# Performance work log

Measured on AMD Instinct MI355X. Metric: run time of the kernel, lower is better.

## Reference

```python
import jax, jax.numpy as jnp
import numpy as np

B, CIN, T, H, W = 4, 64, 8, 32, 32
COUT, AHID = 64, 16
HWF = H * W


def _conv2d(x, w, b):
    y = jax.lax.conv_general_dilated(x, w, (1, 1), [(1, 1), (1, 1)],
                                     dimension_numbers=("NCHW", "OIHW", "NCHW"))
    return y + b[None, :, None, None]


def _conv1x1(x, w, b):
    return jnp.einsum("bchw,oc->bohw", x, w) + b[None, :, None, None]


def setup_inputs():
    key = jax.random.key(0)
    ks = jax.random.split(key, 18)
    s = 0.05
    d = {}
    d["X"] = jax.random.normal(ks[0], (B, CIN, T, H, W), jnp.float32)
    d["conv_w"] = jax.random.normal(ks[1], (4 * COUT, CIN + COUT, 3, 3), jnp.float32) * s
    d["conv_b"] = jnp.zeros((4 * COUT,), jnp.float32)
    d["W_ci"] = jax.random.normal(ks[2], (COUT, H, W), jnp.float32) * s
    d["W_cf"] = jax.random.normal(ks[3], (COUT, H, W), jnp.float32) * s
    d["W_co"] = jax.random.normal(ks[4], (COUT, H, W), jnp.float32) * s
    d["q_w"] = jax.random.normal(ks[5], (AHID, COUT), jnp.float32) * s
    d["q_b"] = jnp.zeros((AHID,), jnp.float32)
    d["k_w"] = jax.random.normal(ks[6], (AHID, COUT), jnp.float32) * s
    d["k_b"] = jnp.zeros((AHID,), jnp.float32)
    d["k2_w"] = jax.random.normal(ks[7], (AHID, COUT), jnp.float32) * s
    d["k2_b"] = jnp.zeros((AHID,), jnp.float32)
    d["v_w"] = jax.random.normal(ks[8], (COUT, COUT), jnp.float32) * s
    d["v_b"] = jnp.zeros((COUT,), jnp.float32)
    d["v2_w"] = jax.random.normal(ks[9], (COUT, COUT), jnp.float32) * s
    d["v2_b"] = jnp.zeros((COUT,), jnp.float32)
    d["z_w"] = jax.random.normal(ks[10], (2 * COUT, 2 * COUT), jnp.float32) * s
    d["z_b"] = jnp.zeros((2 * COUT,), jnp.float32)
    d["m_w"] = jax.random.normal(ks[11], (3 * COUT, 3 * COUT), jnp.float32) * s
    d["m_b"] = jnp.zeros((3 * COUT,), jnp.float32)
    return d


def _forward(X, conv_w, conv_b, W_ci, W_cf, W_co, q_w, q_b, k_w, k_b, k2_w, k2_b,
             v_w, v_b, v2_w, v2_b, z_w, z_b, m_w, m_b):
    def step(carry, x_t):
        h, c, m = carry
        # ConvLSTM cell with peephole connections
        gates = _conv2d(jnp.concatenate([x_t, h], axis=1), conv_w, conv_b)
        i_c, f_c, g_c, o_c = jnp.split(gates, 4, axis=1)
        ig = jax.nn.sigmoid(i_c + W_ci * c)
        fg = jax.nn.sigmoid(f_c + W_cf * c)
        c_new = fg * c + ig * jnp.tanh(g_c)
        og = jax.nn.sigmoid(o_c + W_co * c_new)
        h_new = og * jnp.tanh(c_new)
        # Self-attention memory module (all projections are 1x1 convs)
        q = _conv1x1(h_new, q_w, q_b).reshape(B, AHID, HWF)
        kh = _conv1x1(h_new, k_w, k_b).reshape(B, AHID, HWF)
        vh = _conv1x1(h_new, v_w, v_b).reshape(B, COUT, HWF)
        km = _conv1x1(m, k2_w, k2_b).reshape(B, AHID, HWF)
        vm = _conv1x1(m, v2_w, v2_b).reshape(B, COUT, HWF)
        att_h = jax.nn.softmax(jnp.einsum("ban,bam->bnm", q, kh), axis=-1)  # (B,HW,HW)
        att_m = jax.nn.softmax(jnp.einsum("ban,bam->bnm", q, km), axis=-1)
        z_h = jnp.einsum("bnm,bcm->bcn", att_h, vh)  # (B,COUT,HW)
        z_m = jnp.einsum("bnm,bcm->bcn", att_m, vm)
        z = jnp.concatenate([z_h, z_m], axis=1).reshape(B, 2 * COUT, H, W)
        z = _conv1x1(z, z_w, z_b)
        comb = _conv1x1(jnp.concatenate([z, h_new], axis=1), m_w, m_b)
        mo, mg, mi = jnp.split(comb, 3, axis=1)
        gi = jax.nn.sigmoid(mi)
        m_new = (1.0 - gi) * m + gi * jnp.tanh(mg)
        h_out = jax.nn.sigmoid(mo) * m_new
        return (h_out, c_new, m_new), h_out

    zeros = jnp.zeros((B, COUT, H, W), X.dtype)
    Xs = jnp.moveaxis(X, 2, 0)  # (T, B, CIN, H, W)
    _, hs = jax.lax.scan(step, (zeros, zeros, zeros), Xs)
    return jnp.moveaxis(hs, 0, 2)  # (B, COUT, T, H, W)


def reference(X, conv_w, conv_b, W_ci, W_cf, W_co, q_w, q_b, k_w, k_b, k2_w, k2_b,
              v_w, v_b, v2_w, v2_b, z_w, z_b, m_w, m_b):
    return _forward(X, conv_w, conv_b, W_ci, W_cf, W_co, q_w, q_b, k_w, k_b,
                    k2_w, k2_b, v_w, v_b, v2_w, v2_b, z_w, z_b, m_w, m_b)
```

## Files before the change

### kernel.cpp

```cpp
#include <hip/hip_runtime.h>
#include <hip/hip_bf16.h>

typedef __hip_bfloat16 bf16;
typedef unsigned short ushort;
typedef __attribute__((ext_vector_type(8))) short short8v;
typedef __attribute__((ext_vector_type(4))) float float4v;

__device__ __forceinline__ float b2f(bf16 v){ return __bfloat162float(v); }
__device__ __forceinline__ float sigm(float x){ return 1.0f/(1.0f+__expf(-x)); }
__device__ __forceinline__ float tanhc(float x){
  x = fminf(15.0f, fmaxf(-15.0f, x));
  float e = __expf(2.0f*x);
  return (e-1.0f)/(e+1.0f);
}
__device__ __forceinline__ ushort f2bu(float f){
  bf16 h = __float2bfloat16(f); return *reinterpret_cast<ushort*>(&h);
}
__device__ __forceinline__ float bu2f(ushort u){
  return __uint_as_float(((unsigned)u)<<16);
}
__device__ __forceinline__ short8v ldfrag(const ushort* p){
  return *reinterpret_cast<const short8v*>(p);
}
__device__ __forceinline__ void glds16(const ushort* g, ushort* l){
// ... 112 lines not shown

__global__ __launch_bounds__(256) void k_init(const void* __restrict__ conv_w,
                                              const int* __restrict__ flagp,
                                              float* __restrict__ ws){
  int i = blockIdx.x*256 + threadIdx.x;
  int flag = *flagp;
  if (i < 786432) ws[WS_H + i] = 0.0f;
  if (i < 32) ws[WS_ZROW + i] = 0.0f;
  if (i < 196608) ((unsigned*)(ws + WS_QB16))[i] = 0u;
  if (i < 294912){
    int ci = i & 127;
    int j = i >> 7;
    int mm = j & 255, p = j >> 8;
    int cc = mm >> 2, g = mm & 3;
    int si = ((g*64 + cc)*128 + ci)*9 + p;
    float f;
    ushort hi, lo = 0;
    if (flag){
      f = ((const float*)conv_w)[si];
      hi = f2bu(f);
      lo = f2bu(f - bu2f(hi));
    } else {
      hi = ((const ushort*)conv_w)[si];
    }
    if (ci < 64){
      int di = (j << 6) + ((((ci >> 3) ^ (mm & 7)) << 3) | (ci & 7));
      ((ushort*)(ws + WS_WXAH))[di] = hi;
      ((ushort*)(ws + WS_WXAL))[di] = lo;
    } else {
      int c2 = ci - 64;
      int di = (j << 6) + ((((c2 >> 3) ^ (mm & 7)) << 3) | (c2 & 7));
      ((ushort*)(ws + WS_WHAH))[di] = hi;
      ((ushort*)(ws + WS_WHAL))[di] = lo;
    }
  }
  if (i < 131072){
    ((unsigned*)(ws + WS_HTHI))[i] = 0u;
    ((unsigned*)(ws + WS_HTLO))[i] = 0u;
    ((unsigned*)(ws + WS_MTH))[i] = 0u;
    ((unsigned*)(ws + WS_MTL))[i] = 0u;
  }
}

__global__ __launch_bounds__(256) void k_xt(const void* __restrict__ Xraw,
                                            const int* __restrict__ flagp,
                                            float* __restrict__ ws){
  __shared__ ushort hi_s[64][66];
  __shared__ ushort lo_s[64][66];
  int pt = blockIdx.x, s = blockIdx.y;
  int b = s >> 3, t = s & 7;
  int flag = *flagp;
  int tid = threadIdx.x;
  for (int k = 0; k < 16; ++k){
    int idx = tid + k*256;
    int ci = idx >> 6, pxl = idx & 63;
    size_t si = ((size_t)(b*64 + ci)*8 + t)*1024 + pt*64 + pxl;
    if (flag){
      float f = ((const float*)Xraw)[si];
      ushort h = f2bu(f);
      hi_s[pxl][ci] = h;
      lo_s[pxl][ci] = f2bu(f - bu2f(h));
    } else {
      hi_s[pxl][ci] = ((const ushort*)Xraw)[si];
    }
  }
  __syncthreads();
  ushort* xh = (ushort*)(ws + WS_XTHI) + ((size_t)s*1024 + pt*64)*64;
  ushort* xl = (ushort*)(ws + WS_XTLO) + ((size_t)s*1024 + pt*64)*64;
  for (int k = 0; k < 16; ++k){
    int idx = tid + k*256;
    int pxl = idx >> 6, ci = idx & 63;
    xh[pxl*64 + ci] = hi_s[pxl][ci];
    if (flag) xl[pxl*64 + ci] = lo_s[pxl][ci];
  }
}

__global__ __launch_bounds__(512, 4) void k_convx(
  const int* __restrict__ flagp,
  const ushort* __restrict__ wxah, const ushort* __restrict__ wxal,
  const ushort* __restrict__ xt_hi, const ushort* __restrict__ xt_lo,
  float* __restrict__ gxg, ushort* __restrict__ gxo)
{
  __shared__ ushort xabuf[8192];
  __shared__ ushort xsm[54*136];
  int nt = blockIdx.x, mh = blockIdx.y, tb = blockIdx.z;
  int tid = threadIdx.x;
  int flag = *flagp;
  int ytile = nt >> 1, x0 = (nt & 1) * 16;
  const ushort* xb  = xt_hi + (size_t)tb*65536;
  const ushort* xlb = xt_lo + (size_t)tb*65536;
  int w = tid >> 6, lane = tid & 63, lr = lane & 15, lk = lane >> 4;
  const ushort* aw  = wxah + (size_t)(mh*128 + w*16)*64 + lane*8;
  const ushort* awl = wxal + (size_t)(mh*128 + w*16)*64 + lane*8;
  ushort* areg = xabuf + w*1024;

  const uint4 Z16 = make_uint4(0,0,0,0);
  for (int idx = tid; idx < 864; idx += 512){
    int slot = idx >> 4, c = idx & 15;
    int rr = slot / 18, xi = slot - rr*18;
    int gy = ytile - 1 + rr, gx2 = x0 - 1 + xi;
    bool valid = (gy >= 0) & (gy < 32) & (gx2 >= 0) & (gx2 < 32);
    int px = gy*32 + gx2;
    uint4 v = Z16;
    if (valid){
      if (c < 8)       v = *reinterpret_cast<const uint4*>(xb  + (size_t)px*64 + c*8);
      else if (flag)   v = *reinterpret_cast<const uint4*>(xlb + (size_t)px*64 + (c-8)*8);
    }
    *reinterpret_cast<uint4*>(&xsm[slot*136 + c*8]) = v;
  }
  __syncthreads();

  int px = nt*16 + lr;
  int sw = lr & 7;
  const int cx0 = ((lk ^ sw) << 3);
  const int cx1 = (((4+lk) ^ sw) << 3);
  float4v acc = {0.f,0.f,0.f,0.f};

  #pragma unroll 1
  for (int p = 0; p < 9; ++p){
    glds16(aw + (size_t)p*16384,       areg);
    glds16(aw + (size_t)p*16384 + 512, areg + 512);
    asm volatile("s_waitcnt vmcnt(0)" ::: "memory");
    __builtin_amdgcn_sched_barrier(0);
    short8v A0 = ldfrag(areg + lr*64 + cx0);
    short8v A1 = ldfrag(areg + lr*64 + cx1);
    int pinl = (p/3)*18 + lr + (p%3);
    const ushort* bl = &xsm[pinl*136 + lk*8];
    short8v BX0 = ldfrag(bl), BX1 = ldfrag(bl+32);
    acc = __builtin_amdgcn_mfma_f32_16x16x32_bf16(A0, BX0, acc, 0,0,0);
    acc = __builtin_amdgcn_mfma_f32_16x16x32_bf16(A1, BX1, acc, 0,0,0);
    if (flag){
      short8v BXl0 = ldfrag(bl+64), BXl1 = ldfrag(bl+96);
      acc = __builtin_amdgcn_mfma_f32_16x16x32_bf16(A0, BXl0, acc, 0,0,0);
      acc = __builtin_amdgcn_mfma_f32_16x16x32_bf16(A1, BXl1, acc, 0,0,0);
      asm volatile("s_waitcnt lgkmcnt(0)" ::: "memory");
      __builtin_amdgcn_sched_barrier(0);
      glds16(awl + (size_t)p*16384,       areg);
      glds16(awl + (size_t)p*16384 + 512, areg + 512);
      asm volatile("s_waitcnt vmcnt(0)" ::: "memory");
      __builtin_amdgcn_sched_barrier(0);
      short8v Al0 = ldfrag(areg + lr*64 + cx0);
      short8v Al1 = ldfrag(areg + lr*64 + cx1);
      acc = __builtin_amdgcn_mfma_f32_16x16x32_bf16(Al0, BX0, acc, 0,0,0);
      acc = __builtin_amdgcn_mfma_f32_16x16x32_bf16(Al1, BX1, acc, 0,0,0);
      asm volatile("s_waitcnt lgkmcnt(0)" ::: "memory");
      __builtin_amdgcn_sched_barrier(0);
    } else {
      asm volatile("s_waitcnt lgkmcnt(0)" ::: "memory");
      __builtin_amdgcn_sched_barrier(0);
    }
  }

  {
    int cc = mh*32 + w*4 + lk;
    gxg[((size_t)tb*64 + cc)*1024 + px] = acc[2];
    ushort* go = gxo + ((size_t)tb*192 + cc*3)*1024 + px;
    go[0]    = f2bu(acc[0]);
    go[1024] = f2bu(acc[1]);
    go[2048] = f2bu(acc[3]);
  }
}

__global__ __launch_bounds__(512, 4) void k_conv_mfma(
  const int* __restrict__ flagp,
  const ushort* __restrict__ whah, const ushort* __restrict__ whal,
  const ushort* __restrict__ ht_hi, const ushort* __restrict__ ht_lo,
  const float* __restrict__ gxg, const ushort* __restrict__ gxo,
  const float* __restrict__ smalls, float* __restrict__ cst,
  ushort* __restrict__ hnth, ushort* __restrict__ hntl, int t)
{
  __shared__ ushort albuf[16384];
  __shared__ ushort bsm[54*136];
  int nt = blockIdx.x, mh = blockIdx.y, b = blockIdx.z;
  int tid = threadIdx.x;
  int flag = *flagp;
  int ytile = nt >> 1, x0 = (nt & 1) * 16;

  const ushort* hb  = ht_hi + (size_t)b*65536;
  const ushort* hlb = ht_lo + (size_t)b*65536;

  int w = tid >> 6, lane = tid & 63, lr = lane & 15, lk = lane >> 4;
  const ushort* aw  = whah + (size_t)(mh*128 + w*16)*64 + lane*8;
  const ushort* awl = whal + (size_t)(mh*128 + w*16)*64 + lane*8;
  ushort* areg = albuf + w*1024;
  ushort* aregl = albuf + 8192 + w*1024;

  if (!flag){
    glds16(aw, areg);
    glds16(aw + 512, areg + 512);
  }

  int px = nt*16 + lr;
  int cc = mh*32 + w*4 + lk;
  int tb = b*8 + t;
  const ushort* go = gxo + ((size_t)tb*192 + cc*3)*1024 + px;
  float a0 = bu2f(go[0]);
  float a1 = bu2f(go[1024]);
  float a3 = bu2f(go[2048]);
  float a2 = gxg[((size_t)tb*64 + cc)*1024 + px];

  const uint4 Z16 = make_uint4(0,0,0,0);
  for (int idx = tid; idx < 864; idx += 512){
    int slot = idx >> 4, c = idx & 15;
    int rr = slot / 18, xi = slot - rr*18;
    int gy = ytile - 1 + rr, gx2 = x0 - 1 + xi;
    bool valid = (gy >= 0) & (gy < 32) & (gx2 >= 0) & (gx2 < 32);
    int hpx = gy*32 + gx2;
    uint4 v = Z16;
    if (valid){
      if (c < 8) v = *reinterpret_cast<const uint4*>(hb  + (size_t)hpx*64 + c*8);
      else       v = *reinterpret_cast<const uint4*>(hlb + (size_t)hpx*64 + (c-8)*8);
    }
    *reinterpret_cast<uint4*>(&bsm[slot*136 + c*8]) = v;
  }
  __syncthreads();

  const int sw = lr & 7;
  const int c2n = ((lk ^ sw) << 3);
  const int c3n = (((4+lk) ^ sw) << 3);

  float4v acc = {a0, a1, a2, a3};

  if (!flag){
    #pragma unroll
    for (int p = 0; p < 9; ++p){
      if (p > 0){
        asm volatile("s_waitcnt vmcnt(0)" ::: "memory");
        __builtin_amdgcn_sched_barrier(0);
      }
      short8v A2 = ldfrag(areg + lr*64 + c2n);
      short8v A3 = ldfrag(areg + lr*64 + c3n);
      if (p < 8){
        asm volatile("s_waitcnt lgkmcnt(0)" ::: "memory");
        __builtin_amdgcn_sched_barrier(0);
        glds16(aw + (size_t)(p+1)*16384,       areg);
        glds16(aw + (size_t)(p+1)*16384 + 512, areg + 512);
        __builtin_amdgcn_sched_barrier(0);
      }
      int pinl = (p/3)*18 + lr + (p%3);
      const ushort* bl = &bsm[pinl*136 + lk*8];
      short8v BH0 = ldfrag(bl),    BH1 = ldfrag(bl+32);
      short8v BL0 = ldfrag(bl+64), BL1 = ldfrag(bl+96);
      acc = __builtin_amdgcn_mfma_f32_16x16x32_bf16(A2, BH0, acc, 0,0,0);
      acc = __builtin_amdgcn_mfma_f32_16x16x32_bf16(A3, BH1, acc, 0,0,0);
      acc = __builtin_amdgcn_mfma_f32_16x16x32_bf16(A2, BL0, acc, 0,0,0);
      acc = __builtin_amdgcn_mfma_f32_16x16x32_bf16(A3, BL1, acc, 0,0,0);
    }
  } else {
    #pragma unroll 1
    for (int p = 0; p < 9; ++p){
      glds16(aw + (size_t)p*16384,       areg);
      glds16(aw + (size_t)p*16384 + 512, areg + 512);
      glds16(awl + (size_t)p*16384,       aregl);
      glds16(awl + (size_t)p*16384 + 512, aregl + 512);
      asm volatile("s_waitcnt vmcnt(0)" ::: "memory");
      __builtin_amdgcn_sched_barrier(0);
      short8v A2 = ldfrag(areg + lr*64 + c2n);
      short8v A3 = ldfrag(areg + lr*64 + c3n);
      short8v Al2 = ldfrag(aregl + lr*64 + c2n);
      short8v Al3 = ldfrag(aregl + lr*64 + c3n);
      int pinl = (p/3)*18 + lr + (p%3);
      const ushort* bl = &bsm[pinl*136 + lk*8];
      short8v BH0 = ldfrag(bl),    BH1 = ldfrag(bl+32);
      short8v BL0 = ldfrag(bl+64), BL1 = ldfrag(bl+96);
      acc = __builtin_amdgcn_mfma_f32_16x16x32_bf16(A2, BH0, acc, 0,0,0);
      acc = __builtin_amdgcn_mfma_f32_16x16x32_bf16(A3, BH1, acc, 0,0,0);
      acc = __builtin_amdgcn_mfma_f32_16x16x32_bf16(A2, BL0, acc, 0,0,0);
      acc = __builtin_amdgcn_mfma_f32_16x16x32_bf16(A3, BL1, acc, 0,0,0);
      acc = __builtin_amdgcn_mfma_f32_16x16x32_bf16(Al2, BH0, acc, 0,0,0);
      acc = __builtin_amdgcn_mfma_f32_16x16x32_bf16(Al3, BH1, acc, 0,0,0);
      asm volatile("s_waitcnt lgkmcnt(0)" ::: "memory");
      __builtin_amdgcn_sched_barrier(0);
    }
  }

  {
    int wi = cc*1024 + px;
    size_t sidx = ((size_t)(b*64 + cc))*1024 + px;
    float cprev = cst[sidx];
    float ic = acc[0] + smalls[O_CB + cc];
    float fc = acc[1] + smalls[O_CB + 64 + cc];
    float gc = acc[2] + smalls[O_CB + 128 + cc];
    float oc = acc[3] + smalls[O_CB + 192 + cc];
    float ig = sigm(ic + smalls[O_WCI + wi]*cprev);
    float fg = sigm(fc + smalls[O_WCF + wi]*cprev);
    float cnew = fg*cprev + ig*tanhc(gc);
    float og = sigm(oc + smalls[O_WCO + wi]*cnew);
    cst[sidx] = cnew;
    float hv = og*tanhc(cnew);
    size_t tix = ((size_t)b*1024 + px)*64 + cc;
    ushort hh = f2bu(hv);
    hnth[tix] = hh;
    hntl[tix] = f2bu(hv - bu2f(hh));
  }
}

__global__ __launch_bounds__(256) void k_projm(
  const ushort* __restrict__ hnth, const ushort* __restrict__ hntl,
  const ushort* __restrict__ mth, const ushort* __restrict__ mtl,
  const ushort* __restrict__ pwh, const ushort* __restrict__ pwl,
  const float* __restrict__ smalls, const int* __restrict__ flagp,
  ushort* __restrict__ qb16, ushort* __restrict__ khb16, ushort* __restrict__ kmb16,
  ushort* __restrict__ vth16, ushort* __restrict__ vtm16)
{
  int nt = blockIdx.x, b = blockIdx.y;
  int n0 = nt*16;
  int tid = threadIdx.x;
  int w = tid >> 6, lane = tid & 63, lr = lane & 15, lk = lane >> 4;
  int flag = *flagp;
  const float4v Z4 = {0.f,0.f,0.f,0.f};
  size_t bb = ((size_t)b*1024 + n0 + lr)*64 + lk*8;
  short8v BH0  = ldfrag(hnth + bb), BH1  = ldfrag(hnth + bb + 32);
  short8v BHl0 = ldfrag(hntl + bb), BHl1 = ldfrag(hntl + bb + 32);
  short8v BM0  = ldfrag(mth + bb),  BM1  = ldfrag(mth + bb + 32);
  short8v BMl0 = ldfrag(mtl + bb),  BMl1 = ldfrag(mtl + bb + 32);
  int n = n0 + lr;
  int tstart = w*3;
  int tcnt = (w == 3) ? 2 : 3;
  for (int ti = 0; ti < tcnt; ++ti){
    int tt = tstart + ti;
    const ushort* ar = pwh + (size_t)(tt*16 + lr)*64 + lk*8;
    short8v a0 = ldfrag(ar), a1 = ldfrag(ar + 32);
    bool srcm = (tt == 2) || (tt >= 7);
    short8v b0  = srcm ? BM0  : BH0,  b1  = srcm ? BM1  : BH1;
    short8v bl0 = srcm ? BMl0 : BHl0, bl1 = srcm ? BMl1 : BHl1;
    float4v d = Z4;
    d = __builtin_amdgcn_mfma_f32_16x16x32_bf16(a0, b0,  d, 0,0,0);
    d = __builtin_amdgcn_mfma_f32_16x16x32_bf16(a1, b1,  d, 0,0,0);
    d = __builtin_amdgcn_mfma_f32_16x16x32_bf16(a0, bl0, d, 0,0,0);
    d = __builtin_amdgcn_mfma_f32_16x16x32_bf16(a1, bl1, d, 0,0,0);
    if (flag){
      const ushort* arl = pwl + (size_t)(tt*16 + lr)*64 + lk*8;
      short8v al0 = ldfrag(arl), al1 = ldfrag(arl + 32);
      d = __builtin_amdgcn_mfma_f32_16x16x32_bf16(al0, b0, d, 0,0,0);
      d = __builtin_amdgcn_mfma_f32_16x16x32_bf16(al1, b1, d, 0,0,0);
    }
    int boff = (tt==0) ? O_QB : (tt==1) ? O_KB : (tt==2) ? O_K2B
             : (tt<7) ? (O_VB + (tt-3)*16) : (O_V2B + (tt-7)*16);
    if (tt < 3){
      ushort* base = (tt==0) ? qb16 : (tt==1) ? khb16 : kmb16;
      ushort u[4];
      #pragma unroll
      for (int q = 0; q < 4; ++q)
        u[q] = f2bu(d[q] + smalls[boff + lk*4 + q]);
      *reinterpret_cast<uint2*>(&base[((size_t)b*1024 + n)*32 + lk*4]) =
        make_uint2((unsigned)u[0] | ((unsigned)u[1]<<16),
                   (unsigned)u[2] | ((unsigned)u[3]<<16));
    } else {
      ushort* base = (tt<7) ? vth16 : vtm16;
      int cc0 = ((tt<7) ? (tt-3) : (tt-7))*16 + lk*4;
      #pragma unroll
      for (int q = 0; q < 4; ++q)
        base[((size_t)b*64 + cc0 + q)*1024 + n] = f2bu(d[q] + smalls[boff + lk*4 + q]);
    }
  }
}

__global__ __launch_bounds__(512) void k_fattz(
  const ushort* __restrict__ qb16, const ushort* __restrict__ khb16,
  const ushort* __restrict__ kmb16, const ushort* __restrict__ vth16,
  const ushort* __restrict__ vtm16,
  const ushort* __restrict__ hnth, const ushort* __restrict__ hntl,
  const float* __restrict__ smalls,
  const ushort* __restrict__ zw16h, const ushort* __restrict__ zw16l,
  const ushort* __restrict__ mw16h, const ushort* __restrict__ mw16l,
  const int* __restrict__ flagp,
  float* __restrict__ mst, ushort* __restrict__ mth, ushort* __restrict__ mtl,
  ushort* __restrict__ hth, ushort* __restrict__ htl,
  void* __restrict__ outraw, int t)
{
  __shared__ __align__(16) unsigned char poolA[17408];
  __shared__ __align__(16) ushort ztbh[16*136];
  __shared__ __align__(16) ushort ztbl[16*136];
  __shared__ float cb[192*17];
  __shared__ float ml[64*17];
  __shared__ float rs_s[2][4][16];

  ushort* es   = (ushort*)poolA;
  ushort* zbh  = (ushort*)poolA;
  ushort* zbl  = (ushort*)(poolA + 8704);
  float*  ho_s = (float*)poolA;
  float*  mn_s = (float*)(poolA + 4352);

  int nt = blockIdx.x, b = blockIdx.y;
  int n0 = nt*16;
  int tid = threadIdx.x;
  int w = tid >> 6, lane = tid & 63, lr = lane & 15, lk = lane >> 4;
  int br = w >> 2, wq = w & 3;
  int flag = *flagp;
  const float4v Z4 = {0.f,0.f,0.f,0.f};

  const ushort* kb = (br ? kmb16 : khb16) + (size_t)b*32768;
  const ushort* vt = (br ? vtm16 : vth16) + (size_t)b*65536;
  const ushort* qp = qb16 + (size_t)b*32768;
  ushort* esb = es + br*4352;

  for (int idx = tid; idx < 1024; idx += 512){
    int ch = idx >> 4, pp = idx & 15;
    ml[ch*17+pp] = mst[((size_t)b*64 + ch)*1024 + n0 + pp];
  }

  short8v qf = ldfrag(qp + (size_t)(n0 + lr)*32 + lk*8);

  float4v acc[2];
  acc[0]=Z4; acc[1]=Z4;
  float rsum = 0.f;

  #pragma unroll 1
  for (int mc = 0; mc < 4; ++mc){
    int mbase = mc*256 + wq*64;
    #pragma unroll
    for (int tau = 0; tau < 4; ++tau){
      short8v af = ldfrag(kb + (size_t)(mbase + tau*16 + lr)*32 + lk*8);
      float4v d = __builtin_amdgcn_mfma_f32_16x16x32_bf16(af, qf, Z4, 0,0,0);
      ushort u0 = f2bu(__expf(fminf(d[0], 60.f)));
      ushort u1 = f2bu(__expf(fminf(d[1], 60.f)));
      ushort u2 = f2bu(__expf(fminf(d[2], 60.f)));
      ushort u3 = f2bu(__expf(fminf(d[3], 60.f)));
      rsum += (bu2f(u0) + bu2f(u1)) + (bu2f(u2) + bu2f(u3));
// ... 126 lines not shown
    for (int q = 0; q < 4; ++q)
      cb[(r0+q)*17 + lr] = cacc[q] + smalls[O_MB + r0 + q];
  }
  __syncthreads();

  {
    int px = tid >> 5, lr2 = tid & 31;
    #pragma unroll
    for (int j = 0; j < 2; ++j){
      int ch = lr2 + 32*j;
      float mo = cb[ch*17 + px];
      float mg = cb[(64+ch)*17 + px];
      float mi = cb[(128+ch)*17 + px];
      float mold = ml[ch*17 + px];
      float gi = sigm(mi);
      float mnew = (1.0f-gi)*mold + gi*tanhc(mg);
      float ho = sigm(mo)*mnew;
      ho_s[ch*17+px] = ho;
      mn_s[ch*17+px] = mnew;
    }
  }
  __syncthreads();
  for (int idx = tid; idx < 1024; idx += 512){
    int ch = idx >> 4, pp = idx & 15;
    int n = n0 + pp;
    size_t gidx = ((size_t)b*64 + ch)*1024 + n;
    float mn = mn_s[ch*17+pp];
    mst[gidx] = mn;
    float ho = ho_s[ch*17+pp];
    size_t tix = ((size_t)b*1024 + n)*64 + ch;
    ushort hb_ = f2bu(ho);
    hth[tix] = hb_;
    htl[tix] = f2bu(ho - bu2f(hb_));
    ushort mh_ = f2bu(mn);
    mth[tix] = mh_;
    mtl[tix] = f2bu(mn - bu2f(mh_));
    size_t oidx = ((size_t)(b*64+ch)*8 + t)*1024 + n;
    if (flag) ((float*)outraw)[oidx] = ho;
    else      ((bf16*)outraw)[oidx] = __float2bfloat16(ho);
  }
}

extern "C" void kernel_launch(void* const* d_in, const int* in_sizes, int n_in,
                              void* d_out, int out_size, void* d_ws, size_t ws_size,
                              hipStream_t stream)
{
  float* ws = (float*)d_ws;
  int* flag = (int*)(ws + WS_FLAG);
  float* c    = ws + WS_C;
  float* m    = ws + WS_M;
  float* gxg  = ws + WS_GXG;
  ushort* gxo   = (ushort*)(ws + WS_GXO);
  ushort* qb16  = (ushort*)(ws + WS_QB16);
  ushort* khb16 = (ushort*)(ws + WS_KHB16);
  ushort* kmb16 = (ushort*)(ws + WS_KMB16);
  ushort* vth16 = (ushort*)(ws + WS_VTH16);
  ushort* vtm16 = (ushort*)(ws + WS_VTM16);
  ushort* mth   = (ushort*)(ws + WS_MTH);
  ushort* mtl   = (ushort*)(ws + WS_MTL);
  ushort* hnth  = (ushort*)(ws + WS_HNTH);
  ushort* hntl  = (ushort*)(ws + WS_HNTL);
  ushort* zw16h = (ushort*)(ws + WS_ZW16H);
  ushort* zw16l = (ushort*)(ws + WS_ZW16L);
  ushort* mw16h = (ushort*)(ws + WS_MW16H);
  ushort* mw16l = (ushort*)(ws + WS_MW16L);
  ushort* wxah  = (ushort*)(ws + WS_WXAH);
  ushort* wxal  = (ushort*)(ws + WS_WXAL);
  ushort* whah  = (ushort*)(ws + WS_WHAH);
  ushort* whal  = (ushort*)(ws + WS_WHAL);
  ushort* xt_hi = (ushort*)(ws + WS_XTHI);
  ushort* xt_lo = (ushort*)(ws + WS_XTLO);
  ushort* ht_hi = (ushort*)(ws + WS_HTHI);
  ushort* ht_lo = (ushort*)(ws + WS_HTLO);
  ushort* pwh   = (ushort*)(ws + WS_PWH);
  ushort* pwl   = (ushort*)(ws + WS_PWL);

  k_probe<<<1, 256, 0, stream>>>((const unsigned int*)d_in[0], flag);
  P18 pk;
  for (int i = 0; i < 18; ++i) pk.p[i] = d_in[2 + i];
  k_wconv<<<dim3(64,18), 256, 0, stream>>>(pk, flag, ws);
  k_init<<<3072, 256, 0, stream>>>(d_in[1], flag, ws);
  k_xt<<<dim3(16,32), 256, 0, stream>>>(d_in[0], flag, ws);
  k_wtrans<<<144, 256, 0, stream>>>(ws);
  k_convx<<<dim3(64,2,32), 512, 0, stream>>>(flag, wxah, wxal, xt_hi, xt_lo, gxg, gxo);

  for (int t = 0; t < 8; ++t){
    k_conv_mfma<<<dim3(64,2,4), 512, 0, stream>>>(flag, whah, whal, ht_hi, ht_lo,
                                                  gxg, gxo, ws, c, hnth, hntl, t);
    k_projm<<<dim3(64,4), 256, 0, stream>>>(hnth, hntl, mth, mtl, pwh, pwl, ws, flag,
                                            qb16, khb16, kmb16, vth16, vtm16);
    k_fattz<<<dim3(64,4), 512, 0, stream>>>(qb16, khb16, kmb16, vth16, vtm16,
                                            hnth, hntl, ws, zw16h, zw16l, mw16h, mw16l,
                                            flag, m, mth, mtl, ht_hi, ht_lo, d_out, t);
  }
  (void)in_sizes; (void)n_in; (void)out_size; (void)ws_size;
}
```

Before: 421.9 us.

## Batch four frames per block in input conv and double-buffer recurrent weight loads

The input-side conv kernel now handles four (batch,time) frames per block. Each weight fragment is loaded once and reused across four accumulators, and the grid shrinks from 32 to 8 in z. The recurrent conv kernel's bf16-only path switches to a two-buffer weight prefetch with a partial vmcnt wait, so global-to-LDS loads overlap the MFMAs. The larger LDS footprint and fewer blocks may cut occupancy and parallelism for the one-shot input conv.

```diff
diff --git a/kernel.cpp b/kernel.cpp
--- a/kernel.cpp
+++ b/kernel.cpp
@@ -218,82 +218,147 @@
   float* __restrict__ gxg, ushort* __restrict__ gxo)
 {
   __shared__ ushort xabuf[8192];
-  __shared__ ushort xsm[54*136];
-  int nt = blockIdx.x, mh = blockIdx.y, tb = blockIdx.z;
+  __shared__ ushort xsm4[15552];
+  int nt = blockIdx.x, mh = blockIdx.y, btg = blockIdx.z;
   int tid = threadIdx.x;
   int flag = *flagp;
   int ytile = nt >> 1, x0 = (nt & 1) * 16;
-  const ushort* xb  = xt_hi + (size_t)tb*65536;
-  const ushort* xlb = xt_lo + (size_t)tb*65536;
   int w = tid >> 6, lane = tid & 63, lr = lane & 15, lk = lane >> 4;
   const ushort* aw  = wxah + (size_t)(mh*128 + w*16)*64 + lane*8;
   const ushort* awl = wxal + (size_t)(mh*128 + w*16)*64 + lane*8;
   ushort* areg = xabuf + w*1024;
 
-  const uint4 Z16 = make_uint4(0,0,0,0);
-  for (int idx = tid; idx < 864; idx += 512){
-    int slot = idx >> 4, c = idx & 15;
-    int rr = slot / 18, xi = slot - rr*18;
-    int gy = ytile - 1 + rr, gx2 = x0 - 1 + xi;
-    bool valid = (gy >= 0) & (gy < 32) & (gx2 >= 0) & (gx2 < 32);
-    int px = gy*32 + gx2;
-    uint4 v = Z16;
-    if (valid){
-      if (c < 8)       v = *reinterpret_cast<const uint4*>(xb  + (size_t)px*64 + c*8);
-      else if (flag)   v = *reinterpret_cast<const uint4*>(xlb + (size_t)px*64 + (c-8)*8);
-    }
-    *reinterpret_cast<uint4*>(&xsm[slot*136 + c*8]) = v;
-  }
-  __syncthreads();
-
   int px = nt*16 + lr;
   int sw = lr & 7;
   const int cx0 = ((lk ^ sw) << 3);
   const int cx1 = (((4+lk) ^ sw) << 3);
-  float4v acc = {0.f,0.f,0.f,0.f};
-
-  #pragma unroll 1
-  for (int p = 0; p < 9; ++p){
-    glds16(aw + (size_t)p*16384,       areg);
-    glds16(aw + (size_t)p*16384 + 512, areg + 512);
-    asm volatile("s_waitcnt vmcnt(0)" ::: "memory");
-    __builtin_amdgcn_sched_barrier(0);
-    short8v A0 = ldfrag(areg + lr*64 + cx0);
-    short8v A1 = ldfrag(areg + lr*64 + cx1);
-    int pinl = (p/3)*18 + lr + (p%3);
-    const ushort* bl = &xsm[pinl*136 + lk*8];
-    short8v BX0 = ldfrag(bl), BX1 = ldfrag(bl+32);
-    acc = __builtin_amdgcn_mfma_f32_16x16x32_bf16(A0, BX0, acc, 0,0,0);
-    acc = __builtin_amdgcn_mfma_f32_16x16x32_bf16(A1, BX1, acc, 0,0,0);
-    if (flag){
-      short8v BXl0 = ldfrag(bl+64), BXl1 = ldfrag(bl+96);
-      acc = __builtin_amdgcn_mfma_f32_16x16x32_bf16(A0, BXl0, acc, 0,0,0);
-      acc = __builtin_amdgcn_mfma_f32_16x16x32_bf16(A1, BXl1, acc, 0,0,0);
-      asm volatile("s_waitcnt lgkmcnt(0)" ::: "memory");
-      __builtin_amdgcn_sched_barrier(0);
-      glds16(awl + (size_t)p*16384,       areg);
-      glds16(awl + (size_t)p*16384 + 512, areg + 512);
-      asm volatile("s_waitcnt vmcnt(0)" ::: "memory");
-      __builtin_amdgcn_sched_barrier(0);
-      short8v Al0 = ldfrag(areg + lr*64 + cx0);
-      short8v Al1 = ldfrag(areg + lr*64 + cx1);
-      acc = __builtin_amdgcn_mfma_f32_16x16x32_bf16(Al0, BX0, acc, 0,0,0);
-      acc = __builtin_amdgcn_mfma_f32_16x16x32_bf16(Al1, BX1, acc, 0,0,0);
-      asm volatile("s_waitcnt lgkmcnt(0)" ::: "memory");
-      __builtin_amdgcn_sched_barrier(0);
-    } else {
-      asm volatile("s_waitcnt lgkmcnt(0)" ::: "memory");
-      __builtin_amdgcn_sched_barrier(0);
-    }
-  }
-
-  {
+  const uint4 Z16 = make_uint4(0,0,0,0);
+  const float4v Z4 = {0.f,0.f,0.f,0.f};
+
+  if (!flag){
+    glds16(aw, areg);
+    glds16(aw + 512, areg + 512);
+
+    for (int idx = tid; idx < 1728; idx += 512){
+      int j = idx / 432, rem = idx - j*432;
+      int slot = rem >> 3, c = rem & 7;
+      int rr = slot / 18, xi = slot - rr*18;
+      int gy = ytile - 1 + rr, gx2 = x0 - 1 + xi;
+      bool valid = (gy >= 0) & (gy < 32) & (gx2 >= 0) & (gx2 < 32);
+      int hp = gy*32 + gx2;
+      const ushort* xb = xt_hi + (size_t)(btg*4 + j)*65536;
+      uint4 v = valid ? *reinterpret_cast<const uint4*>(xb + (size_t)hp*64 + c*8) : Z16;
+      *reinterpret_cast<uint4*>(&xsm4[(j*54 + slot)*72 + c*8]) = v;
+    }
+    __syncthreads();
+
+    float4v acc0 = Z4, acc1 = Z4, acc2 = Z4, acc3 = Z4;
+    #pragma unroll
+    for (int p = 0; p < 9; ++p){
+      if (p > 0){
+        asm volatile("s_waitcnt vmcnt(0)" ::: "memory");
+        __builtin_amdgcn_sched_barrier(0);
+      }
+      short8v A0 = ldfrag(areg + lr*64 + cx0);
+      short8v A1 = ldfrag(areg + lr*64 + cx1);
+      if (p < 8){
+        asm volatile("s_waitcnt lgkmcnt(0)" ::: "memory");
+        __builtin_amdgcn_sched_barrier(0);
+        glds16(aw + (size_t)(p+1)*16384,       areg);
+        glds16(aw + (size_t)(p+1)*16384 + 512, areg + 512);
+        __builtin_amdgcn_sched_barrier(0);
+      }
+      int pinl = (p/3)*18 + lr + (p%3);
+      {
+        const ushort* bl = &xsm4[(0*54 + pinl)*72 + lk*8];
+        acc0 = __builtin_amdgcn_mfma_f32_16x16x32_bf16(A0, ldfrag(bl),    acc0, 0,0,0);
+        acc0 = __builtin_amdgcn_mfma_f32_16x16x32_bf16(A1, ldfrag(bl+32), acc0, 0,0,0);
+      }
+      {
+        const ushort* bl = &xsm4[(1*54 + pinl)*72 + lk*8];
+        acc1 = __builtin_amdgcn_mfma_f32_16x16x32_bf16(A0, ldfrag(bl),    acc1, 0,0,0);
+        acc1 = __builtin_amdgcn_mfma_f32_16x16x32_bf16(A1, ldfrag(bl+32), acc1, 0,0,0);
+      }
+      {
+        const ushort* bl = &xsm4[(2*54 + pinl)*72 + lk*8];
+        acc2 = __builtin_amdgcn_mfma_f32_16x16x32_bf16(A0, ldfrag(bl),    acc2, 0,0,0);
+        acc2 = __builtin_amdgcn_mfma_f32_16x16x32_bf16(A1, ldfrag(bl+32), acc2, 0,0,0);
+      }
+      {
+        const ushort* bl = &xsm4[(3*54 + pinl)*72 + lk*8];
+        acc3 = __builtin_amdgcn_mfma_f32_16x16x32_bf16(A0, ldfrag(bl),    acc3, 0,0,0);
+        acc3 = __builtin_amdgcn_mfma_f32_16x16x32_bf16(A1, ldfrag(bl+32), acc3, 0,0,0);
+      }
+    }
+
     int cc = mh*32 + w*4 + lk;
-    gxg[((size_t)tb*64 + cc)*1024 + px] = acc[2];
-    ushort* go = gxo + ((size_t)tb*192 + cc*3)*1024 + px;
-    go[0]    = f2bu(acc[0]);
-    go[1024] = f2bu(acc[1]);
-    go[2048] = f2bu(acc[3]);
+    #pragma unroll
+    for (int j = 0; j < 4; ++j){
+      float4v a = (j==0) ? acc0 : (j==1) ? acc1 : (j==2) ? acc2 : acc3;
+      int tb = btg*4 + j;
+      gxg[((size_t)tb*64 + cc)*1024 + px] = a[2];
+      ushort* go = gxo + ((size_t)tb*192 + cc*3)*1024 + px;
+      go[0]    = f2bu(a[0]);
+      go[1024] = f2bu(a[1]);
+      go[2048] = f2bu(a[3]);
+    }
+  } else {
+    for (int j = 0; j < 4; ++j){
+      int tb = btg*4 + j;
+      const ushort* xb  = xt_hi + (size_t)tb*65536;
+      const ushort* xlb = xt_lo + (size_t)tb*65536;
+      __syncthreads();
+      for (int idx = tid; idx < 864; idx += 512){
+        int slot = idx >> 4, c = idx & 15;
+        int rr = slot / 18, xi = slot - rr*18;
+        int gy = ytile - 1 + rr, gx2 = x0 - 1 + xi;
+        bool valid = (gy >= 0) & (gy < 32) & (gx2 >= 0) & (gx2 < 32);
+        int hp = gy*32 + gx2;
+        uint4 v = Z16;
+        if (valid){
+          if (c < 8) v = *reinterpret_cast<const uint4*>(xb  + (size_t)hp*64 + c*8);
+          else       v = *reinterpret_cast<const uint4*>(xlb + (size_t)hp*64 + (c-8)*8);
+        }
+        *reinterpret_cast<uint4*>(&xsm4[slot*136 + c*8]) = v;
+      }
+      __syncthreads();
+      float4v acc = Z4;
+      #pragma unroll 1
+      for (int p = 0; p < 9; ++p){
+        glds16(aw + (size_t)p*16384,       areg);
+        glds16(aw + (size_t)p*16384 + 512, areg + 512);
+        asm volatile("s_waitcnt vmcnt(0)" ::: "memory");
+        __builtin_amdgcn_sched_barrier(0);
+        short8v A0 = ldfrag(areg + lr*64 + cx0);
+        short8v A1 = ldfrag(areg + lr*64 + cx1);
+        int pinl = (p/3)*18 + lr + (p%3);
+        const ushort* bl = &xsm4[pinl*136 + lk*8];
+        short8v BX0 = ldfrag(bl), BX1 = ldfrag(bl+32);
+        acc = __builtin_amdgcn_mfma_f32_16x16x32_bf16(A0, BX0, acc, 0,0,0);
+        acc = __builtin_amdgcn_mfma_f32_16x16x32_bf16(A1, BX1, acc, 0,0,0);
+        short8v BXl0 = ldfrag(bl+64), BXl1 = ldfrag(bl+96);
+        acc = __builtin_amdgcn_mfma_f32_16x16x32_bf16(A0, BXl0, acc, 0,0,0);
+        acc = __builtin_amdgcn_mfma_f32_16x16x32_bf16(A1, BXl1, acc, 0,0,0);
+        asm volatile("s_waitcnt lgkmcnt(0)" ::: "memory");
+        __builtin_amdgcn_sched_barrier(0);
+        glds16(awl + (size_t)p*16384,       areg);
+        glds16(awl + (size_t)p*16384 + 512, areg + 512);
+        asm volatile("s_waitcnt vmcnt(0)" ::: "memory");
+        __builtin_amdgcn_sched_barrier(0);
+        short8v Al0 = ldfrag(areg + lr*64 + cx0);
+        short8v Al1 = ldfrag(areg + lr*64 + cx1);
+        acc = __builtin_amdgcn_mfma_f32_16x16x32_bf16(Al0, BX0, acc, 0,0,0);
+        acc = __builtin_amdgcn_mfma_f32_16x16x32_bf16(Al1, BX1, acc, 0,0,0);
+        asm volatile("s_waitcnt lgkmcnt(0)" ::: "memory");
+        __builtin_amdgcn_sched_barrier(0);
+      }
+      int cc = mh*32 + w*4 + lk;
+      gxg[((size_t)tb*64 + cc)*1024 + px] = acc[2];
+      ushort* go = gxo + ((size_t)tb*192 + cc*3)*1024 + px;
+      go[0]    = f2bu(acc[0]);
+      go[1024] = f2bu(acc[1]);
+      go[2048] = f2bu(acc[3]);
+    }
   }
 }
 
@@ -318,12 +383,12 @@
   int w = tid >> 6, lane = tid & 63, lr = lane & 15, lk = lane >> 4;
   const ushort* aw  = whah + (size_t)(mh*128 + w*16)*64 + lane*8;
   const ushort* awl = whal + (size_t)(mh*128 + w*16)*64 + lane*8;
-  ushort* areg = albuf + w*1024;
-  ushort* aregl = albuf + 8192 + w*1024;
+  ushort* buf0 = albuf + w*1024;
+  ushort* buf1 = albuf + 8192 + w*1024;
 
   if (!flag){
-    glds16(aw, areg);
-    glds16(aw + 512, areg + 512);
+    glds16(aw, buf0);
+    glds16(aw + 512, buf0 + 512);
   }
 
   int px = nt*16 + lr;
@@ -360,19 +425,18 @@
   if (!flag){
     #pragma unroll
     for (int p = 0; p < 9; ++p){
-      if (p > 0){
+      if (p < 8){
+        ushort* dst = (p & 1) ? buf0 : buf1;
+        glds16(aw + (size_t)(p+1)*16384,       dst);
+        glds16(aw + (size_t)(p+1)*16384 + 512, dst + 512);
+        asm volatile("s_waitcnt vmcnt(2)" ::: "memory");
+      } else {
         asm volatile("s_waitcnt vmcnt(0)" ::: "memory");
-        __builtin_amdgcn_sched_barrier(0);
-      }
-      short8v A2 = ldfrag(areg + lr*64 + c2n);
-      short8v A3 = ldfrag(areg + lr*64 + c3n);
-      if (p < 8){
-        asm volatile("s_waitcnt lgkmcnt(0)" ::: "memory");
-        __builtin_amdgcn_sched_barrier(0);
-        glds16(aw + (size_t)(p+1)*16384,       areg);
-        glds16(aw + (size_t)(p+1)*16384 + 512, areg + 512);
-        __builtin_amdgcn_sched_barrier(0);
-      }
+      }
+      __builtin_amdgcn_sched_barrier(0);
+      const ushort* ab = (p & 1) ? buf1 : buf0;
+      short8v A2 = ldfrag(ab + lr*64 + c2n);
+      short8v A3 = ldfrag(ab + lr*64 + c3n);
       int pinl = (p/3)*18 + lr + (p%3);
       const ushort* bl = &bsm[pinl*136 + lk*8];
       short8v BH0 = ldfrag(bl),    BH1 = ldfrag(bl+32);
@@ -385,16 +449,16 @@
   } else {
     #pragma unroll 1
     for (int p = 0; p < 9; ++p){
-      glds16(aw + (size_t)p*16384,       areg);
-      glds16(aw + (size_t)p*16384 + 512, areg + 512);
-      glds16(awl + (size_t)p*16384,       aregl);
-      glds16(awl + (size_t)p*16384 + 512, aregl + 512);
+      glds16(aw + (size_t)p*16384,       buf0);
+      glds16(aw + (size_t)p*16384 + 512, buf0 + 512);
+      glds16(awl + (size_t)p*16384,       buf1);
+      glds16(awl + (size_t)p*16384 + 512, buf1 + 512);
       asm volatile("s_waitcnt vmcnt(0)" ::: "memory");
       __builtin_amdgcn_sched_barrier(0);
-      short8v A2 = ldfrag(areg + lr*64 + c2n);
-      short8v A3 = ldfrag(areg + lr*64 + c3n);
-      short8v Al2 = ldfrag(aregl + lr*64 + c2n);
-      short8v Al3 = ldfrag(aregl + lr*64 + c3n);
+      short8v A2 = ldfrag(buf0 + lr*64 + c2n);
+      short8v A3 = ldfrag(buf0 + lr*64 + c3n);
+      short8v Al2 = ldfrag(buf1 + lr*64 + c2n);
+      short8v Al3 = ldfrag(buf1 + lr*64 + c3n);
       int pinl = (p/3)*18 + lr + (p%3);
       const ushort* bl = &bsm[pinl*136 + lk*8];
       short8v BH0 = ldfrag(bl),    BH1 = ldfrag(bl+32);
@@ -763,7 +827,7 @@
   k_init<<<3072, 256, 0, stream>>>(d_in[1], flag, ws);
   k_xt<<<dim3(16,32), 256, 0, stream>>>(d_in[0], flag, ws);
   k_wtrans<<<144, 256, 0, stream>>>(ws);
-  k_convx<<<dim3(64,2,32), 512, 0, stream>>>(flag, wxah, wxal, xt_hi, xt_lo, gxg, gxo);
+  k_convx<<<dim3(64,2,8), 512, 0, stream>>>(flag, wxah, wxal, xt_hi, xt_lo, gxg, gxo);
 
   for (int t = 0; t < 8; ++t){
     k_conv_mfma<<<dim3(64,2,4), 512, 0, stream>>>(flag, whah, whal, ht_hi, ht_lo,
```

New measurement: 438.8 us. 1.04x slower.

## Fuse recurrent conv and q/k/v projection into one 1024-thread kernel

Applied to the files above, without the earlier changes.

Merges the per-step recurrent ConvLSTM conv kernel and the projection kernel into a single launch. Each block now covers all 64 output channels of a 16-pixel tile with 16 waves, so the new h goes to shared memory and feeds the q/k/v projections directly instead of being re-read from global memory by a separate kernel. This removes one launch per timestep and halves the conv grid. The trade-offs are that the low-part weight buffer is dropped and the flag path serialises the hi/lo weight loads through one buffer, and the 1024-thread blocks may reduce occupancy.

```diff
diff --git a/kernel.cpp b/kernel.cpp
--- a/kernel.cpp
+++ b/kernel.cpp
@@ -297,17 +297,23 @@
   }
 }
 
-__global__ __launch_bounds__(512, 4) void k_conv_mfma(
+__global__ __launch_bounds__(1024, 4) void k_convp(
   const int* __restrict__ flagp,
   const ushort* __restrict__ whah, const ushort* __restrict__ whal,
   const ushort* __restrict__ ht_hi, const ushort* __restrict__ ht_lo,
   const float* __restrict__ gxg, const ushort* __restrict__ gxo,
   const float* __restrict__ smalls, float* __restrict__ cst,
-  ushort* __restrict__ hnth, ushort* __restrict__ hntl, int t)
+  const ushort* __restrict__ pwh, const ushort* __restrict__ pwl,
+  const ushort* __restrict__ mth, const ushort* __restrict__ mtl,
+  ushort* __restrict__ hnth, ushort* __restrict__ hntl,
+  ushort* __restrict__ qb16, ushort* __restrict__ khb16, ushort* __restrict__ kmb16,
+  ushort* __restrict__ vth16, ushort* __restrict__ vtm16, int t)
 {
   __shared__ ushort albuf[16384];
   __shared__ ushort bsm[54*136];
-  int nt = blockIdx.x, mh = blockIdx.y, b = blockIdx.z;
+  __shared__ ushort hbh[16*72];
+  __shared__ ushort hbl[16*72];
+  int nt = blockIdx.x, b = blockIdx.y;
   int tid = threadIdx.x;
   int flag = *flagp;
   int ytile = nt >> 1, x0 = (nt & 1) * 16;
@@ -316,10 +322,9 @@
   const ushort* hlb = ht_lo + (size_t)b*65536;
 
   int w = tid >> 6, lane = tid & 63, lr = lane & 15, lk = lane >> 4;
-  const ushort* aw  = whah + (size_t)(mh*128 + w*16)*64 + lane*8;
-  const ushort* awl = whal + (size_t)(mh*128 + w*16)*64 + lane*8;
+  const ushort* aw  = whah + (size_t)(w*16)*64 + lane*8;
+  const ushort* awl = whal + (size_t)(w*16)*64 + lane*8;
   ushort* areg = albuf + w*1024;
-  ushort* aregl = albuf + 8192 + w*1024;
 
   if (!flag){
     glds16(aw, areg);
@@ -327,7 +332,7 @@
   }
 
   int px = nt*16 + lr;
-  int cc = mh*32 + w*4 + lk;
+  int cc = w*4 + lk;
   int tb = b*8 + t;
   const ushort* go = gxo + ((size_t)tb*192 + cc*3)*1024 + px;
   float a0 = bu2f(go[0]);
@@ -336,8 +341,8 @@
   float a2 = gxg[((size_t)tb*64 + cc)*1024 + px];
 
   const uint4 Z16 = make_uint4(0,0,0,0);
-  for (int idx = tid; idx < 864; idx += 512){
-    int slot = idx >> 4, c = idx & 15;
+  if (tid < 864){
+    int slot = tid >> 4, c = tid & 15;
     int rr = slot / 18, xi = slot - rr*18;
     int gy = ytile - 1 + rr, gx2 = x0 - 1 + xi;
     bool valid = (gy >= 0) & (gy < 32) & (gx2 >= 0) & (gx2 < 32);
@@ -387,14 +392,20 @@
     for (int p = 0; p < 9; ++p){
       glds16(aw + (size_t)p*16384,       areg);
       glds16(aw + (size_t)p*16384 + 512, areg + 512);
-      glds16(awl + (size_t)p*16384,       aregl);
-      glds16(awl + (size_t)p*16384 + 512, aregl + 512);
       asm volatile("s_waitcnt vmcnt(0)" ::: "memory");
       __builtin_amdgcn_sched_barrier(0);
       short8v A2 = ldfrag(areg + lr*64 + c2n);
       short8v A3 = ldfrag(areg + lr*64 + c3n);
-      short8v Al2 = ldfrag(aregl + lr*64 + c2n);
-      short8v Al3 = ldfrag(aregl + lr*64 + c3n);
+      asm volatile("s_waitcnt lgkmcnt(0)" ::: "memory");
+      __builtin_amdgcn_sched_barrier(0);
+      glds16(awl + (size_t)p*16384,       areg);
+      glds16(awl + (size_t)p*16384 + 512, areg + 512);
+      asm volatile("s_waitcnt vmcnt(0)" ::: "memory");
+      __builtin_amdgcn_sched_barrier(0);
+      short8v Al2 = ldfrag(areg + lr*64 + c2n);
+      short8v Al3 = ldfrag(areg + lr*64 + c3n);
+      asm volatile("s_waitcnt lgkmcnt(0)" ::: "memory");
+      __builtin_amdgcn_sched_barrier(0);
       int pinl = (p/3)*18 + lr + (p%3);
       const ushort* bl = &bsm[pinl*136 + lk*8];
       short8v BH0 = ldfrag(bl),    BH1 = ldfrag(bl+32);
@@ -405,8 +416,6 @@
       acc = __builtin_amdgcn_mfma_f32_16x16x32_bf16(A3, BL1, acc, 0,0,0);
       acc = __builtin_amdgcn_mfma_f32_16x16x32_bf16(Al2, BH0, acc, 0,0,0);
       acc = __builtin_amdgcn_mfma_f32_16x16x32_bf16(Al3, BH1, acc, 0,0,0);
-      asm volatile("s_waitcnt lgkmcnt(0)" ::: "memory");
-      __builtin_amdgcn_sched_barrier(0);
     }
   }
 
@@ -426,51 +435,41 @@
     float hv = og*tanhc(cnew);
     size_t tix = ((size_t)b*1024 + px)*64 + cc;
     ushort hh = f2bu(hv);
+    ushort hl2 = f2bu(hv - bu2f(hh));
     hnth[tix] = hh;
-    hntl[tix] = f2bu(hv - bu2f(hh));
-  }
-}
-
-__global__ __launch_bounds__(256) void k_projm(
-  const ushort* __restrict__ hnth, const ushort* __restrict__ hntl,
-  const ushort* __restrict__ mth, const ushort* __restrict__ mtl,
-  const ushort* __restrict__ pwh, const ushort* __restrict__ pwl,
-  const float* __restrict__ smalls, const int* __restrict__ flagp,
-  ushort* __restrict__ qb16, ushort* __restrict__ khb16, ushort* __restrict__ kmb16,
-  ushort* __restrict__ vth16, ushort* __restrict__ vtm16)
-{
-  int nt = blockIdx.x, b = blockIdx.y;
-  int n0 = nt*16;
-  int tid = threadIdx.x;
-  int w = tid >> 6, lane = tid & 63, lr = lane & 15, lk = lane >> 4;
-  int flag = *flagp;
-  const float4v Z4 = {0.f,0.f,0.f,0.f};
-  size_t bb = ((size_t)b*1024 + n0 + lr)*64 + lk*8;
-  short8v BH0  = ldfrag(hnth + bb), BH1  = ldfrag(hnth + bb + 32);
-  short8v BHl0 = ldfrag(hntl + bb), BHl1 = ldfrag(hntl + bb + 32);
-  short8v BM0  = ldfrag(mth + bb),  BM1  = ldfrag(mth + bb + 32);
-  short8v BMl0 = ldfrag(mtl + bb),  BMl1 = ldfrag(mtl + bb + 32);
-  int n = n0 + lr;
-  int tstart = w*3;
-  int tcnt = (w == 3) ? 2 : 3;
-  for (int ti = 0; ti < tcnt; ++ti){
-    int tt = tstart + ti;
+    hntl[tix] = hl2;
+    hbh[lr*72 + cc] = hh;
+    hbl[lr*72 + cc] = hl2;
+  }
+  __syncthreads();
+
+  if (w < 11){
+    int tt = w;
+    const float4v Z4 = {0.f,0.f,0.f,0.f};
+    bool srcm = (tt == 2) || (tt >= 7);
+    short8v b0, b1, bl0, bl1;
+    if (srcm){
+      size_t bb = ((size_t)b*1024 + nt*16 + lr)*64 + lk*8;
+      b0  = ldfrag(mth + bb);  b1  = ldfrag(mth + bb + 32);
+      bl0 = ldfrag(mtl + bb);  bl1 = ldfrag(mtl + bb + 32);
+    } else {
+      b0  = ldfrag(&hbh[lr*72 + lk*8]);  b1  = ldfrag(&hbh[lr*72 + 32 + lk*8]);
+      bl0 = ldfrag(&hbl[lr*72 + lk*8]);  bl1 = ldfrag(&hbl[lr*72 + 32 + lk*8]);
+    }
     const ushort* ar = pwh + (size_t)(tt*16 + lr)*64 + lk*8;
-    short8v a0 = ldfrag(ar), a1 = ldfrag(ar + 32);
-    bool srcm = (tt == 2) || (tt >= 7);
-    short8v b0  = srcm ? BM0  : BH0,  b1  = srcm ? BM1  : BH1;
-    short8v bl0 = srcm ? BMl0 : BHl0, bl1 = srcm ? BMl1 : BHl1;
+    short8v pa0 = ldfrag(ar), pa1 = ldfrag(ar + 32);
     float4v d = Z4;
-    d = __builtin_amdgcn_mfma_f32_16x16x32_bf16(a0, b0,  d, 0,0,0);
-    d = __builtin_amdgcn_mfma_f32_16x16x32_bf16(a1, b1,  d, 0,0,0);
-    d = __builtin_amdgcn_mfma_f32_16x16x32_bf16(a0, bl0, d, 0,0,0);
-    d = __builtin_amdgcn_mfma_f32_16x16x32_bf16(a1, bl1, d, 0,0,0);
+    d = __builtin_amdgcn_mfma_f32_16x16x32_bf16(pa0, b0,  d, 0,0,0);
+    d = __builtin_amdgcn_mfma_f32_16x16x32_bf16(pa1, b1,  d, 0,0,0);
+    d = __builtin_amdgcn_mfma_f32_16x16x32_bf16(pa0, bl0, d, 0,0,0);
+    d = __builtin_amdgcn_mfma_f32_16x16x32_bf16(pa1, bl1, d, 0,0,0);
     if (flag){
       const ushort* arl = pwl + (size_t)(tt*16 + lr)*64 + lk*8;
-      short8v al0 = ldfrag(arl), al1 = ldfrag(arl + 32);
-      d = __builtin_amdgcn_mfma_f32_16x16x32_bf16(al0, b0, d, 0,0,0);
-      d = __builtin_amdgcn_mfma_f32_16x16x32_bf16(al1, b1, d, 0,0,0);
-    }
+      short8v pal0 = ldfrag(arl), pal1 = ldfrag(arl + 32);
+      d = __builtin_amdgcn_mfma_f32_16x16x32_bf16(pal0, b0, d, 0,0,0);
+      d = __builtin_amdgcn_mfma_f32_16x16x32_bf16(pal1, b1, d, 0,0,0);
+    }
+    int n = nt*16 + lr;
     int boff = (tt==0) ? O_QB : (tt==1) ? O_KB : (tt==2) ? O_K2B
              : (tt<7) ? (O_VB + (tt-3)*16) : (O_V2B + (tt-7)*16);
     if (tt < 3){
@@ -766,10 +765,10 @@
   k_convx<<<dim3(64,2,32), 512, 0, stream>>>(flag, wxah, wxal, xt_hi, xt_lo, gxg, gxo);
 
   for (int t = 0; t < 8; ++t){
-    k_conv_mfma<<<dim3(64,2,4), 512, 0, stream>>>(flag, whah, whal, ht_hi, ht_lo,
-                                                  gxg, gxo, ws, c, hnth, hntl, t);
-    k_projm<<<dim3(64,4), 256, 0, stream>>>(hnth, hntl, mth, mtl, pwh, pwl, ws, flag,
-                                            qb16, khb16, kmb16, vth16, vtm16);
+    k_convp<<<dim3(64,4), 1024, 0, stream>>>(flag, whah, whal, ht_hi, ht_lo,
+                                             gxg, gxo, ws, c, pwh, pwl, mth, mtl,
+                                             hnth, hntl, qb16, khb16, kmb16,
+                                             vth16, vtm16, t);
     k_fattz<<<dim3(64,4), 512, 0, stream>>>(qb16, khb16, kmb16, vth16, vtm16,
                                             hnth, hntl, ws, zw16h, zw16l, mw16h, mw16l,
                                             flag, m, mth, mtl, ht_hi, ht_lo, d_out, t);
```

Result: faster. 410.7 us (-2.7%).
